# Performance work log

Hardware: AMD Instinct MI355X
Metric: run time of the kernel (lower is better)

## Reference

```python
import jax, jax.numpy as jnp
import numpy as np
from jax import lax

B, CIN, T = 16, 2, 4096
DM, DI, DS, DR, DC, NL = 128, 256, 16, 8, 4, 6  # d_model, d_inner, d_state, dt_rank, d_conv, n_layers


def setup_inputs():
    ks = iter(jax.random.split(jax.random.key(0), 48))
    def rn(shape, s=0.05):
        return jax.random.normal(next(ks), shape, jnp.float32) * s
    rng = np.random.default_rng(0)
    n_mask = int(round(0.25 / 0.02))
    starts = rng.choice(np.linspace(0.0, 1.0, int(round(1 / 0.02)), endpoint=False), n_mask, replace=False)
    m = np.ones((B, CIN, T), np.float32)
    for s0 in starts:
        m[:, :, int(T * s0):int(T * (s0 + 0.02))] = 0.0
    return {
        'x': jax.random.normal(next(ks), (B, CIN, T), jnp.float32),
        'mask': jnp.asarray(m),
        'enc_W0': rn((32, CIN, 3), 0.3), 'enc_b0': jnp.zeros(32), 'enc_g0': jnp.ones(32), 'enc_be0': jnp.zeros(32),
        'enc_W1': rn((64, 32, 3), 0.1), 'enc_b1': jnp.zeros(64), 'enc_g1': jnp.ones(64), 'enc_be1': jnp.zeros(64),
        'enc_W2': rn((128, 64, 3), 0.08), 'enc_b2': jnp.zeros(128), 'enc_g2': jnp.ones(128), 'enc_be2': jnp.zeros(128),
        'ln_g': jnp.ones((NL, DM)), 'ln_b': jnp.zeros((NL, DM)),
        'in_W': rn((NL, 2 * DI, DM)), 'conv_W': rn((NL, DI, DC), 0.3), 'conv_b': jnp.zeros((NL, DI)),
        'xp_W': rn((NL, DR + 2 * DS, DI)), 'dt_W': rn((NL, DI, DR), 0.2),
        'dt_b': jnp.full((NL, DI), -4.6, jnp.float32),  # softplus -> dt ~ 0.01
        'A_log': jnp.tile(jnp.log(jnp.arange(1, DS + 1, dtype=jnp.float32)), (NL, DI, 1)),
        'D_p': jnp.ones((NL, DI)), 'out_W': rn((NL, DM, DI)),
        'nf_g': jnp.ones(DM), 'nf_b': jnp.zeros(DM),
        'dec_W0': rn((128, 64, 3), 0.08), 'dec_b0': jnp.zeros(64), 'dec_g0': jnp.ones(64), 'dec_be0': jnp.zeros(64),
        'dec_W1': rn((64, 32, 3), 0.1), 'dec_b1': jnp.zeros(32), 'dec_g1': jnp.ones(32), 'dec_be1': jnp.zeros(32),
        'dec_W2': rn((32, CIN, 3), 0.1), 'dec_b2': jnp.zeros(CIN),
    }


def _conv(x, W, b, stride, pad):
    y = lax.conv_general_dilated(x, W, (stride,), [(pad, pad)], dimension_numbers=('NCH', 'OIH', 'NCH'))
    return y + b[None, :, None]


def _deconv(x, W, b, stride=2, pad=1, out_pad=1):
    # torch ConvTranspose1d weight (in, out, k) -> flipped conv with lhs dilation
    k = W.shape[-1]
    Wc = jnp.flip(W, -1).transpose(1, 0, 2)
    y = lax.conv_general_dilated(x, Wc, (1,), [(k - 1 - pad, k - 1 - pad + out_pad)],
                                 lhs_dilation=(stride,), dimension_numbers=('NCH', 'OIH', 'NCH'))
    return y + b[None, :, None]


def _gn1(x, g, b, eps=1e-5):  # GroupNorm(1, C) over (C, L)
    m = x.mean((1, 2), keepdims=True)
    v = ((x - m) ** 2).mean((1, 2), keepdims=True)
    return (x - m) * lax.rsqrt(v + eps) * g[None, :, None] + b[None, :, None]


def _ln(x, g, b, eps=1e-5):
    m = x.mean(-1, keepdims=True)
    v = ((x - m) ** 2).mean(-1, keepdims=True)
    return (x - m) * lax.rsqrt(v + eps) * g + b


def _mamba(u, in_W, conv_W, conv_b, xp_W, dt_W, dt_b, A_log, D_p, out_W):
    # u: (B, L, DM)
    xz = jnp.einsum('bld,ed->ble', u, in_W)            # (B, L, 2*DI)
    xi, z = xz[..., :DI], xz[..., DI:]
    xc = jnp.pad(xi.transpose(0, 2, 1), ((0, 0), (0, 0), (DC - 1, 0)))  # causal pad
    xc = lax.conv_general_dilated(xc, conv_W[:, None, :], (1,), [(0, 0)],
                                  feature_group_count=DI, dimension_numbers=('NCH', 'OIH', 'NCH'))
    xc = jax.nn.silu(xc + conv_b[None, :, None]).transpose(0, 2, 1)     # (B, L, DI)
    dbl = jnp.einsum('bld,ed->ble', xc, xp_W)          # (B, L, DR+2*DS)
    dt = jax.nn.softplus(jnp.einsum('blr,dr->bld', dbl[..., :DR], dt_W) + dt_b)
    Bm = dbl[..., DR:DR + DS]
    Cm = dbl[..., DR + DS:]
    A = -jnp.exp(A_log)                                # (DI, DS)
    dA = jnp.exp(dt[..., None] * A)                    # (B, L, DI, DS)
    dBx = dt[..., None] * Bm[:, :, None, :] * xc[..., None]
    def comb(e1, e2):
        a1, b1 = e1
        a2, b2 = e2
        return a1 * a2, a2 * b1 + b2
    _, h = lax.associative_scan(comb, (dA, dBx), axis=1)  # selective scan over L
    y = jnp.einsum('blds,bls->bld', h, Cm) + D_p * xc
    y = y * jax.nn.silu(z)
    return jnp.einsum('bld,ed->ble', y, out_W)          # (B, L, DM)


def _forward(x, mask, enc_W0, enc_b0, enc_g0, enc_be0, enc_W1, enc_b1, enc_g1, enc_be1,
             enc_W2, enc_b2, enc_g2, enc_be2, ln_g, ln_b, in_W, conv_W, conv_b, xp_W,
             dt_W, dt_b, A_log, D_p, out_W, nf_g, nf_b,
             dec_W0, dec_b0, dec_g0, dec_be0, dec_W1, dec_b1, dec_g1, dec_be1, dec_W2, dec_b2):
    gelu = lambda t: jax.nn.gelu(t, approximate=False)
    h = mask * x
    h = gelu(_gn1(_conv(h, enc_W0, enc_b0, 2, 1), enc_g0, enc_be0))
    h = gelu(_gn1(_conv(h, enc_W1, enc_b1, 2, 1), enc_g1, enc_be1))
    h = gelu(_gn1(_conv(h, enc_W2, enc_b2, 2, 1), enc_g2, enc_be2))
    s = h.transpose(0, 2, 1)                            # (B, L=T/8, DM)
    for i in range(NL):
        s = s + _mamba(_ln(s, ln_g[i], ln_b[i]), in_W[i], conv_W[i], conv_b[i],
                       xp_W[i], dt_W[i], dt_b[i], A_log[i], D_p[i], out_W[i])
    s = _ln(s, nf_g, nf_b)
    d = s.transpose(0, 2, 1)
    d = gelu(_gn1(_deconv(d, dec_W0, dec_b0), dec_g0, dec_be0))
    d = gelu(_gn1(_deconv(d, dec_W1, dec_b1), dec_g1, dec_be1))
    d = _deconv(d, dec_W2, dec_b2)                      # (B, CIN, T), no norm/act on last block
    return d


def reference(x, mask, enc_W0, enc_b0, enc_g0, enc_be0, enc_W1, enc_b1, enc_g1, enc_be1,
              enc_W2, enc_b2, enc_g2, enc_be2, ln_g, ln_b, in_W, conv_W, conv_b, xp_W,
              dt_W, dt_b, A_log, D_p, out_W, nf_g, nf_b,
              dec_W0, dec_b0, dec_g0, dec_be0, dec_W1, dec_b1, dec_g1, dec_be1, dec_W2, dec_b2):
    d = _forward(x, mask, enc_W0, enc_b0, enc_g0, enc_be0, enc_W1, enc_b1, enc_g1, enc_be1,
                 enc_W2, enc_b2, enc_g2, enc_be2, ln_g, ln_b, in_W, conv_W, conv_b, xp_W,
                 dt_W, dt_b, A_log, D_p, out_W, nf_g, nf_b,
                 dec_W0, dec_b0, dec_g0, dec_be0, dec_W1, dec_b1, dec_g1, dec_be1, dec_W2, dec_b2)
    return (d, x, mask)
```

## Files before the change

kernel.cpp:

```cpp
#include <hip/hip_runtime.h>
#include <hip/hip_bf16.h>
#include <math.h>

#define NB 16
#define TT 4096
#define LL 512
#define DM 128
#define DI 256
#define NLAYER 6
#define CL 32
#define NCH 16

typedef __bf16 bf16x8 __attribute__((ext_vector_type(8)));
typedef float f32x4 __attribute__((ext_vector_type(4)));
typedef unsigned short ushort;

static __device__ __forceinline__ float gelu_f(float v){
  return 0.5f*v*(1.f + erff(v*0.70710678118654752f));
}
static __device__ __forceinline__ float silu_f(float v){
  return v/(1.f + __expf(-v));
}
static __device__ __forceinline__ ushort f2b(float v){
  __hip_bfloat16 h = __float2bfloat16(v);
  return *(ushort*)&h;
}

__global__ __launch_bounds__(256) void k_maskmul(const float* __restrict__ x, const float* __restrict__ m,
                          float* __restrict__ out, int n){
  int i = blockIdx.x*256 + threadIdx.x;
  if (i < n) out[i] = x[i]*m[i];
}

__global__ __launch_bounds__(256) void k_castb(const float* __restrict__ in, ushort* __restrict__ out, int n){
  int i = blockIdx.x*256 + threadIdx.x;
  if (i < n) out[i] = f2b(in[i]);
}

__global__ __launch_bounds__(256) void k_conv2(const float* __restrict__ x, const float* __restrict__ W,
                        const float* __restrict__ bias, float* __restrict__ y,
                        int Ci, int Co, int Li, int S){
  __shared__ float w[192];
  int bid = blockIdx.x;
  int ch = bid % S;
  int o  = (bid / S) % Co;
  int b  = bid / (S*Co);
  for (int j = threadIdx.x; j < Ci*3; j += 256) w[j] = W[(size_t)o*Ci*3 + j];
  __syncthreads();
  int Lo = Li >> 1;
  int Lc = Lo / S;
  int t0 = ch*Lc, t1 = t0 + Lc;
  const float* xb = x + (size_t)b*Ci*Li;
  float bo = bias[o];
  float* yo = y + ((size_t)b*Co + o)*Lo;
  for (int t = t0 + threadIdx.x; t < t1; t += 256){
    int tin = 2*t - 1;
    float acc = bo;
    for (int ci = 0; ci < Ci; ci++){
      const float* xr = xb + (size_t)ci*Li;
      float v0 = (tin >= 0) ? xr[tin] : 0.f;
      acc += w[ci*3+0]*v0 + w[ci*3+1]*xr[tin+1] + w[ci*3+2]*xr[tin+2];
    }
    yo[t] = acc;
  }
}

__global__ __launch_bounds__(256) void k_gn_part(const float* __restrict__ x, float* __restrict__ gp){
  int b = blockIdx.x >> 3, k8 = blockIdx.x & 7;
  const float* xb = x + (size_t)b*65536 + (size_t)k8*8192;
  float s = 0.f, s2 = 0.f;
  for (int i = threadIdx.x; i < 8192; i += 256){ float v = xb[i]; s += v; s2 += v*v; }
  #pragma unroll
  for (int o = 32; o; o >>= 1){ s += __shfl_down(s, o); s2 += __shfl_down(s2, o); }
  __shared__ float sh[8];
  int wid = threadIdx.x >> 6;
  if ((threadIdx.x & 63) == 0){ sh[wid] = s; sh[wid+4] = s2; }
  __syncthreads();
  if (threadIdx.x == 0){
    float a = sh[0]+sh[1]+sh[2]+sh[3], a2 = sh[4]+sh[5]+sh[6]+sh[7];
    gp[(b*8+k8)*2+0] = a; gp[(b*8+k8)*2+1] = a2;
  }
}
__global__ __launch_bounds__(256) void k_gn_apply(float* __restrict__ x, const float* __restrict__ g,
                          const float* __restrict__ be, int Tl, const float* __restrict__ gp){
  int gidx = blockIdx.x*256 + threadIdx.x;
  int b = gidx >> 16, i = gidx & 65535;
  float s = 0.f, s2 = 0.f;
  #pragma unroll
  for (int k = 0; k < 8; k++){ s += gp[(b*8+k)*2]; s2 += gp[(b*8+k)*2+1]; }
  float mean = s*(1.f/65536.f);
  float inv  = rsqrtf(s2*(1.f/65536.f) - mean*mean + 1e-5f);
  int c = i / Tl;
  float* p = x + (size_t)b*65536 + i;
  float v = (*p - mean)*inv*g[c] + be[c];
  *p = gelu_f(v);
}

__global__ __launch_bounds__(256) void k_transpose2(const float* __restrict__ in, float* __restrict__ out){
  int idx = blockIdx.x*256 + threadIdx.x;
  if (idx >= NB*DM*LL) return;
  int t = idx & 511;
  int c = (idx >> 9) & 127;
  int b = idx >> 16;
  out[(size_t)b*65536 + (size_t)t*128 + c] = in[idx];
}

__global__ __launch_bounds__(256) void k_transposeB(const float* __restrict__ in, float* __restrict__ out){
  int idx = blockIdx.x*256 + threadIdx.x;
  if (idx >= NB*DM*LL) return;
  int m = idx & 511;
  int c = (idx >> 9) & 127;
  int b = idx >> 16;
  out[idx] = in[(size_t)b*65536 + (size_t)m*128 + c];
}

__global__ __launch_bounds__(256) void k_ln2(const float* __restrict__ x, const float* __restrict__ g,
                      const float* __restrict__ be, float* __restrict__ out, int rows){
  int row = blockIdx.x*4 + (threadIdx.x >> 6);
  if (row >= rows) return;
  int lid = threadIdx.x & 63;
  const float* xr = x + (size_t)row*DM;
  float v0 = xr[lid], v1 = xr[lid+64];
  float s = v0 + v1;
  #pragma unroll
  for (int o = 32; o; o >>= 1) s += __shfl_xor(s, o);
  float mean = s*(1.f/128.f);
  float d0 = v0-mean, d1 = v1-mean;
  float s2 = d0*d0 + d1*d1;
  #pragma unroll
  for (int o = 32; o; o >>= 1) s2 += __shfl_xor(s2, o);
  float inv = rsqrtf(s2*(1.f/128.f) + 1e-5f);
  float* orow = out + (size_t)row*DM;
  orow[lid]    = d0*inv*g[lid]    + be[lid];
  orow[lid+64] = d1*inv*g[lid+64] + be[lid+64];
}

__global__ __launch_bounds__(256) void k_ln2b(const float* __restrict__ x, const float* __restrict__ g,
                      const float* __restrict__ be, ushort* __restrict__ out, int rows){
  int row = blockIdx.x*4 + (threadIdx.x >> 6);
  if (row >= rows) return;
  int lid = threadIdx.x & 63;
  const float* xr = x + (size_t)row*DM;
  float v0 = xr[lid], v1 = xr[lid+64];
  float s = v0 + v1;
  #pragma unroll
  for (int o = 32; o; o >>= 1) s += __shfl_xor(s, o);
  float mean = s*(1.f/128.f);
  float d0 = v0-mean, d1 = v1-mean;
  float s2 = d0*d0 + d1*d1;
  #pragma unroll
  for (int o = 32; o; o >>= 1) s2 += __shfl_xor(s2, o);
  float inv = rsqrtf(s2*(1.f/128.f) + 1e-5f);
  ushort* orow = out + (size_t)row*DM;
  orow[lid]    = f2b(d0*inv*g[lid]    + be[lid]);
  orow[lid+64] = f2b(d1*inv*g[lid+64] + be[lid+64]);
}

template<int ACCUM>
__global__ __launch_bounds__(256) void k_mfma_nt(const ushort* __restrict__ A, const ushort* __restrict__ B,
                          float* __restrict__ C, int N, int K){
  int tid = threadIdx.x;
  int wid = tid >> 6, l = tid & 63;
  int wm = wid >> 1, wn = wid & 1;
  int m0 = blockIdx.y*128 + wm*64;
  int n0 = blockIdx.x*128 + wn*64;
  int lr = l & 15;
  int lk = (l >> 4)*8;
  int orow = (l >> 4)*4;
  f32x4 acc[4][4];
  #pragma unroll
  for (int i = 0; i < 4; i++)
    #pragma unroll
    for (int j = 0; j < 4; j++){
      if (ACCUM){
        #pragma unroll
        for (int r = 0; r < 4; r++)
          acc[i][j][r] = C[(size_t)(m0 + i*16 + orow + r)*N + n0 + j*16 + lr];
      } else {
        acc[i][j] = (f32x4){0.f,0.f,0.f,0.f};
      }
    }
  for (int k0 = 0; k0 < K; k0 += 32){
    bf16x8 a[4], b[4];
    #pragma unroll
    for (int f = 0; f < 4; f++)
      a[f] = *(const bf16x8*)(A + (size_t)(m0 + f*16 + lr)*K + k0 + lk);
    #pragma unroll
    for (int f = 0; f < 4; f++)
      b[f] = *(const bf16x8*)(B + (size_t)(n0 + f*16 + lr)*K + k0 + lk);
    #pragma unroll
    for (int i = 0; i < 4; i++)
      #pragma unroll
      for (int j = 0; j < 4; j++)
        acc[i][j] = __builtin_amdgcn_mfma_f32_16x16x32_bf16(a[i], b[j], acc[i][j], 0, 0, 0);
  }
  #pragma unroll
  for (int i = 0; i < 4; i++)
    #pragma unroll
    for (int j = 0; j < 4; j++)
      #pragma unroll
      for (int r = 0; r < 4; r++)
        C[(size_t)(m0 + i*16 + orow + r)*N + n0 + j*16 + lr] = acc[i][j][r];
}

__global__ __launch_bounds__(256) void k_gemm_xp(const float* __restrict__ A, const float* __restrict__ B,
                          float* __restrict__ C){
  __shared__ float As[32][17];
  __shared__ float Bs[64][17];
  int tid = threadIdx.x;
  int m0 = blockIdx.x*32;
  int tx = tid & 15, ty = tid >> 4;
  float acc[2][4] = {};
  for (int k0 = 0; k0 < 256; k0 += 16){
    if (tid < 128){
      int r = tid >> 2, c = (tid & 3)*4;
      float4 av = *(const float4*)(A + (size_t)(m0+r)*256 + k0 + c);
      As[r][c]=av.x; As[r][c+1]=av.y; As[r][c+2]=av.z; As[r][c+3]=av.w;
    }
    {
      int r = tid >> 2, c = (tid & 3)*4;
      float4 bv = make_float4(0.f,0.f,0.f,0.f);
      if (r < 40) bv = *(const float4*)(B + (size_t)r*256 + k0 + c);
      Bs[r][c]=bv.x; Bs[r][c+1]=bv.y; Bs[r][c+2]=bv.z; Bs[r][c+3]=bv.w;
    }
    __syncthreads();
    #pragma unroll
    for (int k = 0; k < 16; k++){
      float a[2], bb[4];
      #pragma unroll
      for (int i = 0; i < 2; i++) a[i] = As[ty*2+i][k];
      #pragma unroll
      for (int j = 0; j < 4; j++) bb[j] = Bs[tx*4+j][k];
      #pragma unroll
      for (int i = 0; i < 2; i++)
        #pragma unroll
        for (int j = 0; j < 4; j++) acc[i][j] += a[i]*bb[j];
    }
    __syncthreads();
  }
  #pragma unroll
  for (int i = 0; i < 2; i++){
    int m = m0 + ty*2 + i;
    #pragma unroll
    for (int j = 0; j < 4; j++){
      int n = tx*4 + j;
      if (n < 40) C[(size_t)m*40 + n] = acc[i][j];
    }
  }
}

__global__ __launch_bounds__(256) void k_cconv2(const float* __restrict__ xz, const float* __restrict__ cw,
                         const float* __restrict__ cb, float* __restrict__ xc){
  int idx = blockIdx.x*256 + threadIdx.x;
  if (idx >= NB*LL*DI) return;
  int d = idx & 255;
  int l = (idx >> 8) & 511;
  int b = idx >> 17;
  const float* xi = xz + (size_t)b*262144 + d;
  float acc = cb[d];
  #pragma unroll
  for (int j = 0; j < 4; j++){
    int m = l - 3 + j;
    if (m >= 0) acc += xi[(size_t)m*512]*cw[d*4 + j];
  }
  xc[idx] = silu_f(acc);
}

__global__ __launch_bounds__(256) void k_scan_sum(const float* __restrict__ xc, const float* __restrict__ dbl,
                        const float* __restrict__ dtW, const float* __restrict__ dtb,
                        const float* __restrict__ Alog,
                        float* __restrict__ GA, float* __restrict__ GB){
  __shared__ float srow[CL*40];
  int bid = blockIdx.x;
  int b = bid >> 4, ch = bid & 15;
  int d = threadIdx.x;
  const float* dbp = dbl + (size_t)b*20480 + ch*CL*40;
  for (int j = d; j < CL*40; j += 256) srow[j] = dbp[j];
  float4 w0 = *(const float4*)(dtW + d*8);
  float4 w1 = *(const float4*)(dtW + d*8 + 4);
  float tb = dtb[d];
  float a[16];
  #pragma unroll
  for (int s = 0; s < 16; s++) a[s] = -__expf(Alog[d*16 + s]);
  const float* xcp = xc + (size_t)b*131072 + (size_t)ch*CL*256 + d;
  __syncthreads();
  float A[16], Bv[16];
  #pragma unroll
  for (int s = 0; s < 16; s++){ A[s] = 1.f; Bv[s] = 0.f; }
  #pragma unroll
  for (int i = 0; i < CL; i++){
    const float* r = srow + i*40;
    float raw = tb + r[0]*w0.x + r[1]*w0.y + r[2]*w0.z + r[3]*w0.w
                   + r[4]*w1.x + r[5]*w1.y + r[6]*w1.z + r[7]*w1.w;
    float dt = (raw > 20.f) ? raw : log1pf(__expf(raw));
    float xcv = xcp[(size_t)i*256];
    float dxc = dt*xcv;
    #pragma unroll
    for (int s = 0; s < 16; s++){
      float e = __expf(dt*a[s]);
      A[s] *= e;
      Bv[s] = e*Bv[s] + dxc*r[8+s];
    }
  }
  size_t base = (((size_t)b*NCH + ch)*16)*256 + d;
  #pragma unroll
  for (int s = 0; s < 16; s++){
    GA[base + (size_t)s*256] = A[s];
    GB[base + (size_t)s*256] = Bv[s];
  }
}

__global__ __launch_bounds__(256) void k_scan_pre(const float* __restrict__ GA, float* __restrict__ GB){
  int gid = blockIdx.x*256 + threadIdx.x;
  int b = gid >> 12;
  int s = (gid >> 8) & 15;
  int d = gid & 255;
  size_t stride = (size_t)16*256;
  size_t idx = (((size_t)b*NCH)*16 + s)*256 + d;
  float P = 0.f;
  #pragma unroll
  for (int ch = 0; ch < NCH; ch++){
    float Ac = GA[idx], Bc = GB[idx];
    GB[idx] = P;
    P = Ac*P + Bc;
    idx += stride;
  }
}

__global__ __launch_bounds__(256) void k_scan_emit(const float* __restrict__ xc, const float* __restrict__ dbl,
                        const float* __restrict__ xz,
                        const float* __restrict__ dtW, const float* __restrict__ dtb,
                        const float* __restrict__ Alog, const float* __restrict__ Dp,
                        const float* __restrict__ GB, ushort* __restrict__ yb){
  __shared__ float srow[CL*40];
  int bid = blockIdx.x;
  int b = bid >> 4, ch = bid & 15;
  int d = threadIdx.x;
  const float* dbp = dbl + (size_t)b*20480 + ch*CL*40;
  for (int j = d; j < CL*40; j += 256) srow[j] = dbp[j];
  float4 w0 = *(const float4*)(dtW + d*8);
  float4 w1 = *(const float4*)(dtW + d*8 + 4);
  float tb = dtb[d];
  float Dd = Dp[d];
  float a[16];
  #pragma unroll
  for (int s = 0; s < 16; s++) a[s] = -__expf(Alog[d*16 + s]);
  float h[16];
  size_t base = (((size_t)b*NCH + ch)*16)*256 + d;
  #pragma unroll
  for (int s = 0; s < 16; s++) h[s] = GB[base + (size_t)s*256];
  const float* xcp = xc + (size_t)b*131072 + (size_t)ch*CL*256 + d;
  const float* zp = xz + (size_t)b*262144 + (size_t)ch*CL*512 + 256 + d;
  ushort* yp = yb + (size_t)b*131072 + (size_t)ch*CL*256 + d;
  __syncthreads();
  #pragma unroll
  for (int i = 0; i < CL; i++){
    const float* r = srow + i*40;
    float raw = tb + r[0]*w0.x + r[1]*w0.y + r[2]*w0.z + r[3]*w0.w
                   + r[4]*w1.x + r[5]*w1.y + r[6]*w1.z + r[7]*w1.w;
    float dt = (raw > 20.f) ? raw : log1pf(__expf(raw));
    float xcv = xcp[(size_t)i*256];
    float dxc = dt*xcv;
    float y = Dd*xcv;
    #pragma unroll
    for (int s = 0; s < 16; s++){
      float e = __expf(dt*a[s]);
      h[s] = e*h[s] + dxc*r[8+s];
      y += h[s]*r[24+s];
    }
    float zv = zp[(size_t)i*512];
    yp[(size_t)i*256] = f2b(y*silu_f(zv));
  }
}

__global__ __launch_bounds__(256) void k_deconv2p(const float* __restrict__ x, const float* __restrict__ W,
                          const float* __restrict__ bias, float* __restrict__ y,
                          int Ci, int Co, int Li, int cs, int S){
  __shared__ float w[384];
  int bid = blockIdx.x;
  int ch = bid % S;
  int o  = (bid / S) % Co;
  int b  = bid / (S*Co);
  for (int j = threadIdx.x; j < Ci*3; j += 256){
    int i = j/3, k = j - 3*i;
    w[j] = W[((size_t)i*Co + o)*3 + k];
  }
  __syncthreads();
  int Lc = Li / S;
  int m0 = ch*Lc;
  const float* xb = x + (size_t)b*Ci*Li;
  float bo = bias[o];
  float* yo = y + ((size_t)b*Co + o)*(size_t)(2*Li);
  for (int idx = threadIdx.x; idx < Lc; idx += 256){
    int m = m0 + idx;
    float even = bo, odd = bo;
    bool has1 = (m + 1 < Li);
    for (int i = 0; i < Ci; i++){
      const float* xr = xb + (size_t)i*cs;
      float xm  = xr[m];
      float xm1 = has1 ? xr[m+1] : 0.f;
      even += w[i*3+1]*xm;
      odd  += w[i*3+2]*xm + w[i*3+0]*xm1;
    }
    *(float2*)(yo + 2*m) = make_float2(even, odd);
  }
}

__global__ __launch_bounds__(256) void k_copyf(const float* __restrict__ in, float* __restrict__ out, int n){
  int i = blockIdx.x*256 + threadIdx.x;
  if (i < n) out[i] = in[i];
}

extern "C" void kernel_launch(void* const* d_in, const int* in_sizes, int n_in,
                              void* d_out, int out_size, void* d_ws, size_t ws_size,
                              hipStream_t stream) {
  const float* x      = (const float*)d_in[0];
  const float* mask   = (const float*)d_in[1];
  const float* enc_W0 = (const float*)d_in[2];
  const float* enc_b0 = (const float*)d_in[3];
  const float* enc_g0 = (const float*)d_in[4];
  const float* enc_be0= (const float*)d_in[5];
  const float* enc_W1 = (const float*)d_in[6];
  const float* enc_b1 = (const float*)d_in[7];
  const float* enc_g1 = (const float*)d_in[8];
  const float* enc_be1= (const float*)d_in[9];
  const float* enc_W2 = (const float*)d_in[10];
  const float* enc_b2 = (const float*)d_in[11];
  const float* enc_g2 = (const float*)d_in[12];
  const float* enc_be2= (const float*)d_in[13];
  const float* ln_g   = (const float*)d_in[14];
  const float* ln_b   = (const float*)d_in[15];
  const float* in_W   = (const float*)d_in[16];
  const float* conv_W = (const float*)d_in[17];
  const float* conv_b = (const float*)d_in[18];
  const float* xp_W   = (const float*)d_in[19];
  const float* dt_W   = (const float*)d_in[20];
  const float* dt_b   = (const float*)d_in[21];
  const float* A_log  = (const float*)d_in[22];
  const float* D_p    = (const float*)d_in[23];
  const float* out_W  = (const float*)d_in[24];
  const float* nf_g   = (const float*)d_in[25];
  const float* nf_b   = (const float*)d_in[26];
  const float* dec_W0 = (const float*)d_in[27];
  const float* dec_b0 = (const float*)d_in[28];
  const float* dec_g0 = (const float*)d_in[29];
  const float* dec_be0= (const float*)d_in[30];
  const float* dec_W1 = (const float*)d_in[31];
  const float* dec_b1 = (const float*)d_in[32];
  const float* dec_g1 = (const float*)d_in[33];
  const float* dec_be1= (const float*)d_in[34];
  const float* dec_W2 = (const float*)d_in[35];
  const float* dec_b2 = (const float*)d_in[36];

  float* out = (float*)d_out;

  float* ws  = (float*)d_ws;
  float* S    = ws;
  float* U    = S    + 1048576;
  float* XZ   = U    + 1048576;
  float* CBUF = XZ   + 4194304;
  float* GA   = CBUF + 2097152;
  float* GB   = GA   + 1048576;
  float* DBL  = GB   + 1048576;
  float* WBIN = DBL  + 327680;
  float* WBOUT= WBIN + 196608;
  float* EB0 = XZ;
  float* EB1 = XZ + 1048576;
  float* H0  = CBUF;
  float* UT  = CBUF;
  float* GNP = DBL;
  ushort* Ub    = (ushort*)U;
  ushort* Yb    = (ushort*)GA;
  ushort* WbIn  = (ushort*)WBIN;
  ushort* WbOut = (ushort*)WBOUT;

  k_castb<<<1536, 256, 0, stream>>>(in_W,  WbIn,  NLAYER*512*DM);
  k_castb<<<768, 256, 0, stream>>>(out_W, WbOut, NLAYER*DM*DI);

  k_maskmul<<<512, 256, 0, stream>>>(x, mask, H0, NB*2*TT);
  k_conv2<<<16*32*4, 256, 0, stream>>>(H0, enc_W0, enc_b0, EB0, 2, 32, 4096, 4);
  k_gn_part<<<128, 256, 0, stream>>>(EB0, GNP);
  k_gn_apply<<<4096, 256, 0, stream>>>(EB0, enc_g0, enc_be0, 2048, GNP);
  k_conv2<<<16*64*4, 256, 0, stream>>>(EB0, enc_W1, enc_b1, EB1, 32, 64, 2048, 4);
  k_gn_part<<<128, 256, 0, stream>>>(EB1, GNP);
  k_gn_apply<<<4096, 256, 0, stream>>>(EB1, enc_g1, enc_be1, 1024, GNP);
  k_conv2<<<16*128*2, 256, 0, stream>>>(EB1, enc_W2, enc_b2, EB0, 64, 128, 1024, 2);
  k_gn_part<<<128, 256, 0, stream>>>(EB0, GNP);
  k_gn_apply<<<4096, 256, 0, stream>>>(EB0, enc_g2, enc_be2, 512, GNP);
  k_transpose2<<<4096, 256, 0, stream>>>(EB0, S);

  const int rows = NB*LL;
  for (int i = 0; i < NLAYER; i++){
    k_ln2b<<<2048, 256, 0, stream>>>(S, ln_g + i*DM, ln_b + i*DM, Ub, rows);
    k_mfma_nt<0><<<dim3(4, 64), 256, 0, stream>>>(Ub, WbIn + (size_t)i*512*DM, XZ, 512, DM);
    k_cconv2<<<8192, 256, 0, stream>>>(XZ, conv_W + (size_t)i*DI*4, conv_b + (size_t)i*DI, CBUF);
    k_gemm_xp<<<256, 256, 0, stream>>>(CBUF, xp_W + (size_t)i*40*DI, DBL);
    k_scan_sum<<<256, 256, 0, stream>>>(CBUF, DBL,
                                        dt_W + (size_t)i*DI*8, dt_b + (size_t)i*DI,
                                        A_log + (size_t)i*DI*16, GA, GB);
    k_scan_pre<<<256, 256, 0, stream>>>(GA, GB);
    k_scan_emit<<<256, 256, 0, stream>>>(CBUF, DBL, XZ,
                                         dt_W + (size_t)i*DI*8, dt_b + (size_t)i*DI,
                                         A_log + (size_t)i*DI*16, D_p + (size_t)i*DI, GB, Yb);
    k_mfma_nt<1><<<dim3(1, 64), 256, 0, stream>>>(Yb, WbOut + (size_t)i*DM*DI, S, DM, DI);
  }

  k_ln2<<<2048, 256, 0, stream>>>(S, nf_g, nf_b, U, rows);
  k_transposeB<<<4096, 256, 0, stream>>>(U, UT);
  k_deconv2p<<<16*64*2, 256, 0, stream>>>(UT, dec_W0, dec_b0, EB0, 128, 64, 512, 512, 2);
  k_gn_part<<<128, 256, 0, stream>>>(EB0, GNP);
  k_gn_apply<<<4096, 256, 0, stream>>>(EB0, dec_g0, dec_be0, 1024, GNP);
  k_deconv2p<<<16*32*4, 256, 0, stream>>>(EB0, dec_W1, dec_b1, EB1, 64, 32, 1024, 1024, 4);
  k_gn_part<<<128, 256, 0, stream>>>(EB1, GNP);
  k_gn_apply<<<4096, 256, 0, stream>>>(EB1, dec_g1, dec_be1, 2048, GNP);
  k_deconv2p<<<16*2*8, 256, 0, stream>>>(EB1, dec_W2, dec_b2, out, 32, 2, 2048, 2048, 8);

  k_copyf<<<512, 256, 0, stream>>>(x,    out + 131072, 131072);
  k_copyf<<<512, 256, 0, stream>>>(mask, out + 262144, 131072);
}
```

Before: 958.3 us.

## Stage conv/deconv input tiles in LDS and compute all output channels per block

Replaces the per-output-channel encoder convolutions and the first two decoder transposed convolutions with templated kernels. Each block loads an input time tile for all input channels into shared memory, split into even and odd phases for the stride-2 conv, then computes every output channel from it. This removes the repeated global reads of the input that happened once per output channel. In exchange, weights are now read from global memory instead of LDS, and each conv launches only 256 blocks, which is fewer than before.

After: 1.027 ms. +7.2%, slower.

```diff
diff --git a/kernel.cpp b/kernel.cpp
--- a/kernel.cpp
+++ b/kernel.cpp
@@ -37,31 +37,42 @@
   if (i < n) out[i] = f2b(in[i]);
 }
 
-__global__ __launch_bounds__(256) void k_conv2(const float* __restrict__ x, const float* __restrict__ W,
-                        const float* __restrict__ bias, float* __restrict__ y,
-                        int Ci, int Co, int Li, int S){
-  __shared__ float w[192];
+template<int Ci, int Co, int TW>
+__global__ __launch_bounds__(256) void k_conv_lds(const float* __restrict__ x, const float* __restrict__ W,
+                        const float* __restrict__ bias, float* __restrict__ y, int Li){
+  const int Lc = TW;
+  const int Lo = Li >> 1;
+  const int S  = Lo / Lc;
+  __shared__ float xe[Ci][Lc+1];
+  __shared__ float xo[Ci][Lc+1];
   int bid = blockIdx.x;
-  int ch = bid % S;
-  int o  = (bid / S) % Co;
-  int b  = bid / (S*Co);
-  for (int j = threadIdx.x; j < Ci*3; j += 256) w[j] = W[(size_t)o*Ci*3 + j];
+  int b = bid / S, ch = bid % S;
+  int t0 = ch*Lc;
+  const float* xb = x + (size_t)b*Ci*Li;
+  for (int idx = threadIdx.x; idx < Ci*(2*Lc+1); idx += 256){
+    int ci = idx / (2*Lc+1);
+    int j  = idx - ci*(2*Lc+1);
+    int gin = 2*t0 - 1 + j;
+    float v = (gin >= 0 && gin < Li) ? xb[(size_t)ci*Li + gin] : 0.f;
+    if (j & 1) xo[ci][j>>1] = v;
+    else       xe[ci][j>>1] = v;
+  }
   __syncthreads();
-  int Lo = Li >> 1;
-  int Lc = Lo / S;
-  int t0 = ch*Lc, t1 = t0 + Lc;
-  const float* xb = x + (size_t)b*Ci*Li;
-  float bo = bias[o];
-  float* yo = y + ((size_t)b*Co + o)*Lo;
-  for (int t = t0 + threadIdx.x; t < t1; t += 256){
-    int tin = 2*t - 1;
-    float acc = bo;
+  const int NOg = 256/TW;
+  const int OI  = Co/NOg;
+  int tl = threadIdx.x % TW;
+  int og = threadIdx.x / TW;
+  #pragma unroll
+  for (int oi = 0; oi < OI; oi++){
+    int o = oi*NOg + og;
+    const float* w = W + (size_t)o*Ci*3;
+    float acc = bias[o];
+    #pragma unroll 4
     for (int ci = 0; ci < Ci; ci++){
-      const float* xr = xb + (size_t)ci*Li;
-      float v0 = (tin >= 0) ? xr[tin] : 0.f;
-      acc += w[ci*3+0]*v0 + w[ci*3+1]*xr[tin+1] + w[ci*3+2]*xr[tin+2];
-    }
-    yo[t] = acc;
+      float w0 = w[ci*3+0], w1 = w[ci*3+1], w2 = w[ci*3+2];
+      acc += w0*xe[ci][tl] + w1*xo[ci][tl] + w2*xe[ci][tl+1];
+    }
+    y[((size_t)b*Co + o)*Lo + t0 + tl] = acc;
   }
 }
 
@@ -370,6 +381,45 @@
     }
     float zv = zp[(size_t)i*512];
     yp[(size_t)i*256] = f2b(y*silu_f(zv));
+  }
+}
+
+template<int Ci, int Co, int TW>
+__global__ __launch_bounds__(256) void k_deconv_lds(const float* __restrict__ x, const float* __restrict__ W,
+                          const float* __restrict__ bias, float* __restrict__ y, int Li, int cs){
+  const int Lc = TW;
+  const int S  = Li / Lc;
+  __shared__ float xin[Ci][Lc+1];
+  int bid = blockIdx.x;
+  int b = bid / S, ch = bid % S;
+  int m0 = ch*Lc;
+  const float* xb = x + (size_t)b*Ci*Li;
+  for (int idx = threadIdx.x; idx < Ci*(Lc+1); idx += 256){
+    int ci = idx / (Lc+1);
+    int q  = idx - ci*(Lc+1);
+    int m  = m0 + q;
+    xin[ci][q] = (m < Li) ? xb[(size_t)ci*cs + m] : 0.f;
+  }
+  __syncthreads();
+  const int NOg = 256/TW;
+  const int OI  = Co/NOg;
+  int tl = threadIdx.x % TW;
+  int og = threadIdx.x / TW;
+  float* yo = y + (size_t)b*Co*(size_t)(2*Li);
+  #pragma unroll
+  for (int oi = 0; oi < OI; oi++){
+    int o = oi*NOg + og;
+    float bo = bias[o];
+    float even = bo, odd = bo;
+    #pragma unroll 4
+    for (int ci = 0; ci < Ci; ci++){
+      const float* w = W + ((size_t)ci*Co + o)*3;
+      float xm  = xin[ci][tl];
+      float xm1 = xin[ci][tl+1];
+      even += w[1]*xm;
+      odd  += w[2]*xm + w[0]*xm1;
+    }
+    *(float2*)(yo + (size_t)o*(2*Li) + 2*(m0 + tl)) = make_float2(even, odd);
   }
 }
 
@@ -478,13 +528,13 @@
   k_castb<<<768, 256, 0, stream>>>(out_W, WbOut, NLAYER*DM*DI);
 
   k_maskmul<<<512, 256, 0, stream>>>(x, mask, H0, NB*2*TT);
-  k_conv2<<<16*32*4, 256, 0, stream>>>(H0, enc_W0, enc_b0, EB0, 2, 32, 4096, 4);
+  k_conv_lds<2,32,128><<<256, 256, 0, stream>>>(H0, enc_W0, enc_b0, EB0, 4096);
   k_gn_part<<<128, 256, 0, stream>>>(EB0, GNP);
   k_gn_apply<<<4096, 256, 0, stream>>>(EB0, enc_g0, enc_be0, 2048, GNP);
-  k_conv2<<<16*64*4, 256, 0, stream>>>(EB0, enc_W1, enc_b1, EB1, 32, 64, 2048, 4);
+  k_conv_lds<32,64,64><<<256, 256, 0, stream>>>(EB0, enc_W1, enc_b1, EB1, 2048);
   k_gn_part<<<128, 256, 0, stream>>>(EB1, GNP);
   k_gn_apply<<<4096, 256, 0, stream>>>(EB1, enc_g1, enc_be1, 1024, GNP);
-  k_conv2<<<16*128*2, 256, 0, stream>>>(EB1, enc_W2, enc_b2, EB0, 64, 128, 1024, 2);
+  k_conv_lds<64,128,32><<<256, 256, 0, stream>>>(EB1, enc_W2, enc_b2, EB0, 1024);
   k_gn_part<<<128, 256, 0, stream>>>(EB0, GNP);
   k_gn_apply<<<4096, 256, 0, stream>>>(EB0, enc_g2, enc_be2, 512, GNP);
   k_transpose2<<<4096, 256, 0, stream>>>(EB0, S);
@@ -507,10 +557,10 @@
 
   k_ln2<<<2048, 256, 0, stream>>>(S, nf_g, nf_b, U, rows);
   k_transposeB<<<4096, 256, 0, stream>>>(U, UT);
-  k_deconv2p<<<16*64*2, 256, 0, stream>>>(UT, dec_W0, dec_b0, EB0, 128, 64, 512, 512, 2);
+  k_deconv_lds<128,64,32><<<256, 256, 0, stream>>>(UT, dec_W0, dec_b0, EB0, 512, 512);
   k_gn_part<<<128, 256, 0, stream>>>(EB0, GNP);
   k_gn_apply<<<4096, 256, 0, stream>>>(EB0, dec_g0, dec_be0, 1024, GNP);
-  k_deconv2p<<<16*32*4, 256, 0, stream>>>(EB0, dec_W1, dec_b1, EB1, 64, 32, 1024, 1024, 4);
+  k_deconv_lds<64,32,64><<<256, 256, 0, stream>>>(EB0, dec_W1, dec_b1, EB1, 1024, 1024);
   k_gn_part<<<128, 256, 0, stream>>>(EB1, GNP);
   k_gn_apply<<<4096, 256, 0, stream>>>(EB1, dec_g1, dec_be1, 2048, GNP);
   k_deconv2p<<<16*2*8, 256, 0, stream>>>(EB1, dec_W2, dec_b2, out, 32, 2, 2048, 2048, 8);
```
